# Kernel optimization log

Measured on AMD Instinct MI355X. Metric: run time of the kernel, lower is better.

The kernel has to match this reference:

```python
import jax, jax.numpy as jnp
import numpy as np
import math

EMBED_DIM = 1024
NUM_HEADS = 16
HEAD_DIM = EMBED_DIM // NUM_HEADS


def setup_inputs() -> dict:
    key = jax.random.key(0)
    ks = jax.random.split(key, 12)
    B, N = 2, 2048
    s = 1.0 / math.sqrt(EMBED_DIM)
    inp = {
        "query": jax.random.normal(ks[0], (B, N, EMBED_DIM), jnp.float32),
        "key": jax.random.normal(ks[1], (B, N, EMBED_DIM), jnp.float32),
        "value": jax.random.normal(ks[2], (B, N, EMBED_DIM), jnp.float32),
        "Wq": jax.random.normal(ks[3], (EMBED_DIM, EMBED_DIM), jnp.float32) * s,
        "bq": jnp.zeros((EMBED_DIM,), jnp.float32),
        "Wk": jax.random.normal(ks[4], (EMBED_DIM, EMBED_DIM), jnp.float32) * s,
        "bk": jnp.zeros((EMBED_DIM,), jnp.float32),
        "Wv": jax.random.normal(ks[5], (EMBED_DIM, EMBED_DIM), jnp.float32) * s,
        "bv": jnp.zeros((EMBED_DIM,), jnp.float32),
        "Wo": jax.random.normal(ks[6], (EMBED_DIM, EMBED_DIM), jnp.float32) * s,
        "bo": jnp.zeros((EMBED_DIM,), jnp.float32),
        "gate": jnp.zeros((NUM_HEADS,), jnp.float32),
    }
    return inp


def reference(query, key, value, Wq, bq, Wk, bk, Wv, bv, Wo, bo, gate):
    B, Nq, _ = query.shape
    Nk = key.shape[1]
    H, D = NUM_HEADS, HEAD_DIM
    # projections (Linear: x @ W.T + b); split heads -> [B, H, N, D]
    q = (query @ Wq.T + bq).reshape(B, Nq, H, D).transpose(0, 2, 1, 3)
    k = (key @ Wk.T + bk).reshape(B, Nk, H, D).transpose(0, 2, 1, 3)
    v = (value @ Wv.T + bv).reshape(B, Nk, H, D).transpose(0, 2, 1, 3)
    # scaled logits with per-head sigmoid gate folded into the scale
    scale = jax.nn.sigmoid(gate) / math.sqrt(D)  # [H]
    logits = jnp.einsum("bhqd,bhkd->bhqk", q, k) * scale[None, :, None, None]
    attn = jax.nn.softmax(logits, axis=-1)
    out = jnp.einsum("bhqk,bhkd->bhqd", attn, v)
    out = out.transpose(0, 2, 1, 3).reshape(B, Nq, H * D)
    return out @ Wo.T + bo
```

## Files before the change

kernel.cpp:

```cpp
#include <hip/hip_runtime.h>
#include <hip/hip_bf16.h>
#include <cstdint>


#define DEV __device__ __forceinline__
typedef __attribute__((ext_vector_type(8))) short bf16x8;
typedef __attribute__((ext_vector_type(4))) float f32x4;
typedef unsigned short u16;

DEV void async16(const void* g, void* l) {
  __builtin_amdgcn_global_load_lds(
      (const __attribute__((address_space(1))) unsigned int*)g,
      (__attribute__((address_space(3))) unsigned int*)l, 16, 0, 0);
}

DEV u16 bf16_rne(float f) {
  unsigned int u = __builtin_bit_cast(unsigned int, f);
  u += 0x7FFFu + ((u >> 16) & 1u);
  return (u16)(u >> 16);
}

DEV u16 cvt16(float x) {
  __hip_bfloat16 h = __float2bfloat16(x);
  return __builtin_bit_cast(u16, h);
}

DEV unsigned cvtpk(float lo, float hi) {
  unsigned r;
  asm("v_cvt_pk_bf16_f32 %0, %1, %2" : "=v"(r) : "v"(lo), "v"(hi));
  return r;
}

__global__ __launch_bounds__(256) void cast_all(
    const float* __restrict__ q, const float* __restrict__ k, const float* __restrict__ v,
    const float* __restrict__ Wq, const float* __restrict__ Wk,
    const float* __restrict__ Wv, const float* __restrict__ Wo,
    u16* __restrict__ XQ, u16* __restrict__ XK, u16* __restrict__ XV,
    u16* __restrict__ WQB, u16* __restrict__ WKB, u16* __restrict__ WVB,
    u16* __restrict__ WOB) {
  int idx = blockIdx.x * 256 + threadIdx.x;
  const float* src; u16* dst; int i;
  if      (idx <  524288) { src = q;  dst = XQ;  i = idx; }
  else if (idx < 1048576) { src = k;  dst = XK;  i = idx -  524288; }
  else if (idx < 1572864) { src = v;  dst = XV;  i = idx - 1048576; }
  else if (idx < 1703936) { src = Wq; dst = WQB; i = idx - 1572864; }
  else if (idx < 1835008) { src = Wk; dst = WKB; i = idx - 1703936; }
  else if (idx < 1966080) { src = Wv; dst = WVB; i = idx - 1835008; }
  else                    { src = Wo; dst = WOB; i = idx - 1966080; }
  const float4* p = (const float4*)src + (size_t)i * 2;
  float4 a = p[0], b = p[1];
  union { u16 us[8]; uint4 vv; } u;
  u.us[0] = bf16_rne(a.x); u.us[1] = bf16_rne(a.y);
  u.us[2] = bf16_rne(a.z); u.us[3] = bf16_rne(a.w);
  u.us[4] = bf16_rne(b.x); u.us[5] = bf16_rne(b.y);
  u.us[6] = bf16_rne(b.z); u.us[7] = bf16_rne(b.w);
  ((uint4*)dst)[i] = u.vv;
}

__global__ __launch_bounds__(256, 3) void gemm_qkv(
    const u16* __restrict__ XQ, const u16* __restrict__ XK, const u16* __restrict__ XV,
    const u16* __restrict__ Wb,
    const float* __restrict__ bq, const float* __restrict__ bkb, const float* __restrict__ bv,
    const float* __restrict__ gate,
    u16* __restrict__ QB, u16* __restrict__ KB, u16* __restrict__ VTB) {
  __shared__ __attribute__((aligned(16))) u16 As[2][128 * 32];
  __shared__ __attribute__((aligned(16))) u16 Bs[2][128 * 32];
  const int t = threadIdx.x, lane = t & 63, w = t >> 6;
  const int l15 = lane & 15, quad = lane >> 4;
  const int xcd = blockIdx.x & 7, idx = blockIdx.x >> 3;
  const int seg = idx >> 5, r5 = idx & 31;
  const int bm = (xcd << 2) + (r5 >> 3), bn = r5 & 7;
  const int m0 = bm << 7, n0 = bn << 7;
  const u16* A = (seg == 0) ? XQ : (seg == 1) ? XK : XV;
  const u16* W = Wb + (long)seg * 1048576;
  const int wm = (w >> 1) << 6, wn = (w & 1) << 6;
  const int r0 = t >> 2, cc0 = (t & 3) * 8;
  const u16* gA0 = A + (long)(m0 + r0) * 1024 + cc0;
  const u16* gA1 = gA0 + 64 * 1024;
  const u16* gB0 = W + (long)(n0 + r0) * 1024 + cc0;
  const u16* gB1 = gB0 + 64 * 1024;

  async16(gA0, &As[0][t * 8]); async16(gA1, &As[0][(t + 256) * 8]);
  async16(gB0, &Bs[0][t * 8]); async16(gB1, &Bs[0][(t + 256) * 8]);

  f32x4 acc[4][4] = {};
  for (int k0 = 0; k0 < 1024; k0 += 32) {
    const int cur = (k0 >> 5) & 1;
    __syncthreads();
    if (k0 + 32 < 1024) {
      const int kn = k0 + 32, nb = cur ^ 1;
      async16(gA0 + kn, &As[nb][t * 8]); async16(gA1 + kn, &As[nb][(t + 256) * 8]);
      async16(gB0 + kn, &Bs[nb][t * 8]); async16(gB1 + kn, &Bs[nb][(t + 256) * 8]);
    }
    bf16x8 af[4], bfm[4];
#pragma unroll
    for (int i = 0; i < 4; i++)
      af[i] = *(const bf16x8*)&As[cur][(wm + i * 16 + l15) * 32 + quad * 8];
#pragma unroll
    for (int j = 0; j < 4; j++)
      bfm[j] = *(const bf16x8*)&Bs[cur][(wn + j * 16 + l15) * 32 + quad * 8];
#pragma unroll
    for (int i = 0; i < 4; i++)
#pragma unroll
      for (int j = 0; j < 4; j++)
        acc[i][j] = __builtin_amdgcn_mfma_f32_16x16x32_bf16(af[i], bfm[j], acc[i][j], 0, 0, 0);
  }

  if (seg == 2) {
#pragma unroll
    for (int i = 0; i < 4; i++) {
      int token = m0 + wm + i * 16 + quad * 4;
      int bb_ = token >> 11, n = token & 2047;
#pragma unroll
      for (int j = 0; j < 4; j++) {
        int col = n0 + wn + j * 16 + l15;
        float bb = bv[col];
        union { u16 us[4]; uint2 u2; } pk;
#pragma unroll
        for (int r = 0; r < 4; r++) pk.us[r] = bf16_rne(acc[i][j][r] + bb);
        *(uint2*)&VTB[(long)(bb_ * 1024 + col) * 2048 + n] = pk.u2;
      }
    }
  } else {
    const float* bias = seg ? bkb : bq;
    u16* C = seg ? KB : QB;
#pragma unroll
    for (int j = 0; j < 4; j++) {
      int col = n0 + wn + j * 16 + l15;
      float bb = bias[col];
      float scl = 1.f;
      if (seg == 0) {
        float g = gate[col >> 6];
        float sig = 1.f / (1.f + __builtin_amdgcn_exp2f(-g * 1.44269504f));
        scl = sig * 0.125f * 1.44269504f;
      }
#pragma unroll
      for (int i = 0; i < 4; i++) {
        int row = m0 + wm + i * 16 + quad * 4;
#pragma unroll
        for (int r = 0; r < 4; r++)
          C[(long)(row + r) * 1024 + col] = bf16_rne((acc[i][j][r] + bb) * scl);
      }
    }
  }
}

__global__ __launch_bounds__(256, 2) void gemm_out(
    const u16* __restrict__ A, const u16* __restrict__ W,
    const float* __restrict__ bias, float* __restrict__ Cf) {
  __shared__ __attribute__((aligned(16))) u16 As[2][64 * 32];
  __shared__ __attribute__((aligned(16))) u16 Bs[2][128 * 32];
  const int t = threadIdx.x, lane = t & 63, w = t >> 6;
  const int l15 = lane & 15, quad = lane >> 4;
  const int xcd = blockIdx.x & 7, idx = blockIdx.x >> 3;
  const int bm = (xcd << 3) + (idx >> 3), bn = idx & 7;
  const int m0 = bm << 6, n0 = bn << 7;
  const int wm = (w >> 1) << 5, wn = (w & 1) << 6;
  const int r0 = t >> 2, cc0 = (t & 3) * 8;
  const u16* gA = A + (long)(m0 + r0) * 1024 + cc0;
  const u16* gB0 = W + (long)(n0 + r0) * 1024 + cc0;
  const u16* gB1 = gB0 + 64 * 1024;

  async16(gA, &As[0][t * 8]);
  async16(gB0, &Bs[0][t * 8]); async16(gB1, &Bs[0][(t + 256) * 8]);

  f32x4 acc[2][4] = {};
  for (int k0 = 0; k0 < 1024; k0 += 32) {
    const int cur = (k0 >> 5) & 1;
    __syncthreads();
    if (k0 + 32 < 1024) {
      const int kn = k0 + 32, nb = cur ^ 1;
      async16(gA + kn, &As[nb][t * 8]);
      async16(gB0 + kn, &Bs[nb][t * 8]); async16(gB1 + kn, &Bs[nb][(t + 256) * 8]);
    }
    bf16x8 af[2], bfm[4];
#pragma unroll
    for (int i = 0; i < 2; i++)
      af[i] = *(const bf16x8*)&As[cur][(wm + i * 16 + l15) * 32 + quad * 8];
#pragma unroll
    for (int j = 0; j < 4; j++)
      bfm[j] = *(const bf16x8*)&Bs[cur][(wn + j * 16 + l15) * 32 + quad * 8];
#pragma unroll
    for (int i = 0; i < 2; i++)
#pragma unroll
      for (int j = 0; j < 4; j++)
        acc[i][j] = __builtin_amdgcn_mfma_f32_16x16x32_bf16(af[i], bfm[j], acc[i][j], 0, 0, 0);
  }

#pragma unroll
  for (int j = 0; j < 4; j++) {
    int col = n0 + wn + j * 16 + l15;
    float bb = bias[col];
#pragma unroll
    for (int i = 0; i < 2; i++) {
      int row = m0 + wm + i * 16 + quad * 4;
#pragma unroll
      for (int r = 0; r < 4; r++)
        Cf[(long)(row + r) * 1024 + col] = acc[i][j][r] + bb;
    }
  }
}

__global__ __launch_bounds__(128, 5) void attn_kernel(
    const u16* __restrict__ Q, const u16* __restrict__ Kb,
    const u16* __restrict__ Vt, u16* __restrict__ Op0, u16* __restrict__ Op3,
    float* __restrict__ lp) {
  __shared__ __attribute__((aligned(16))) u16 Ks[2][32 * 64];
  __shared__ __attribute__((aligned(16))) u16 Vs[2][64 * 32];
  const int t = threadIdx.x, lane = t & 63, w = t >> 6;
  const int l15 = lane & 15, quad = lane >> 4;
  const int qt = blockIdx.x >> 2, ksp = blockIdx.x & 3;
  const int h = blockIdx.y, b = blockIdx.z;
  const int q0 = qt * 64, tok0 = b * 2048, key0 = ksp * 512;
  const u16* Kbase = Kb + (long)tok0 * 1024 + h * 64;
  const u16* Vbase = Vt + (long)(b * 1024 + h * 64) * 2048 + key0;

  bf16x8 aq[2][2];
#pragma unroll
  for (int i = 0; i < 2; i++) {
    long row = tok0 + q0 + w * 32 + i * 16 + l15;
#pragma unroll
    for (int ks = 0; ks < 2; ks++)
      aq[i][ks] = *(const bf16x8*)&Q[row * 1024 + h * 64 + ks * 32 + quad * 8];
  }

#pragma unroll
  for (int i = 0; i < 2; i++) {
    int c = i * 128 + t;
    int rk = c >> 3, ck = c & 7, cks = ck ^ ((rk >> 1) & 7);
    async16(&Kbase[(long)(key0 + rk) * 1024 + cks * 8], &Ks[0][c * 8]);
    int rv = c >> 2, cv = c & 3, cvs = cv ^ ((rv >> 1) & 3);
    async16(&Vbase[(long)rv * 2048 + cvs * 8], &Vs[0][c * 8]);
  }

  float l_st[2] = {};
  f32x4 O[2][4] = {};

  for (int kt = 0; kt < 16; kt++) {
    const int cur = kt & 1;
    __syncthreads();
    if (kt + 1 < 16) {
      const int kk = (kt + 1) * 32, nb = cur ^ 1;
#pragma unroll
      for (int i = 0; i < 2; i++) {
        int c = i * 128 + t;
        int rk = c >> 3, ck = c & 7, cks = ck ^ ((rk >> 1) & 7);
        async16(&Kbase[(long)(key0 + kk + rk) * 1024 + cks * 8], &Ks[nb][c * 8]);
        int rv = c >> 2, cv = c & 3, cvs = cv ^ ((rv >> 1) & 3);
        async16(&Vbase[(long)rv * 2048 + kk + cvs * 8], &Vs[nb][c * 8]);
      }
    }

    f32x4 s[2][2] = {};
    __builtin_amdgcn_s_setprio(1);
#pragma unroll
    for (int ks = 0; ks < 2; ks++) {
      bf16x8 bk_[2];
#pragma unroll
      for (int j = 0; j < 2; j++) {
        int rl = 2 * l15 + j;
        bk_[j] = *(const bf16x8*)&Ks[cur][rl * 64 + (((ks * 4 + quad) ^ (l15 & 7))) * 8];
      }
#pragma unroll
      for (int i = 0; i < 2; i++)
#pragma unroll
        for (int j = 0; j < 2; j++)
          s[i][j] = __builtin_amdgcn_mfma_f32_16x16x32_bf16(bk_[j], aq[i][ks], s[i][j], 0, 0, 0);
    }
    __builtin_amdgcn_s_setprio(0);

    bf16x8 ap[2];
#pragma unroll
    for (int i = 0; i < 2; i++) {
      union { unsigned uw[4]; bf16x8 v8; } pw;
#pragma unroll
      for (int r = 0; r < 4; r++) {
        float p0 = __builtin_amdgcn_exp2f(s[i][0][r]);
        float p1 = __builtin_amdgcn_exp2f(s[i][1][r]);
        l_st[i] += p0 + p1;
        pw.uw[r] = cvtpk(p0, p1);
      }
      ap[i] = pw.v8;
    }

    bf16x8 bv_[4];
#pragma unroll
    for (int dj = 0; dj < 4; dj++) {
      int rl = dj * 16 + l15;
      bv_[dj] = *(const bf16x8*)&Vs[cur][rl * 32 + ((quad ^ ((rl >> 1) & 3))) * 8];
    }
    __builtin_amdgcn_s_setprio(1);
#pragma unroll
    for (int i = 0; i < 2; i++)
#pragma unroll
      for (int dj = 0; dj < 4; dj++)
        O[i][dj] = __builtin_amdgcn_mfma_f32_16x16x32_bf16(ap[i], bv_[dj], O[i][dj], 0, 0, 0);
    __builtin_amdgcn_s_setprio(0);
  }

  u16* dst = (ksp == 3) ? Op3 : (Op0 + (long)ksp * 4194304);
#pragma unroll
  for (int i = 0; i < 2; i++) {
    float ls = l_st[i];
    ls += __shfl_xor(ls, 16); ls += __shfl_xor(ls, 32);
    if (quad == 0) {
      long qrow = tok0 + q0 + w * 32 + i * 16 + l15;
      lp[ksp * 65536 + (int)qrow * 16 + h] = ls;
    }
#pragma unroll
    for (int r = 0; r < 4; r++) {
      long row = tok0 + q0 + w * 32 + i * 16 + quad * 4 + r;
#pragma unroll
      for (int dj = 0; dj < 4; dj++)
        dst[row * 1024 + h * 64 + dj * 16 + l15] = cvt16(O[i][dj][r]);
    }
  }
}

__global__ __launch_bounds__(256) void merge_kernel(
    const u16* __restrict__ Op0, const u16* __restrict__ Op3,
    const float* __restrict__ lp, u16* __restrict__ AO) {
  int idx = blockIdx.x * 256 + threadIdx.x;
  int tok = idx >> 7, rem = idx & 127, h = rem >> 3;
  int li = tok * 16 + h;
  float inv = 1.f / (lp[li] + lp[65536 + li] + lp[131072 + li] + lp[196608 + li]);
  union U { uint4 v; u16 us[8]; };
  U a0, a1, a2, a3, uo;
  a0.v = ((const uint4*)Op0)[idx];
  a1.v = ((const uint4*)Op0)[idx + 524288];
  a2.v = ((const uint4*)Op0)[idx + 1048576];
  a3.v = ((const uint4*)Op3)[idx];
#pragma unroll
  for (int j = 0; j < 8; j++) {
    float f0 = __builtin_bit_cast(float, (unsigned)((unsigned)a0.us[j] << 16));
    float f1 = __builtin_bit_cast(float, (unsigned)((unsigned)a1.us[j] << 16));
    float f2 = __builtin_bit_cast(float, (unsigned)((unsigned)a2.us[j] << 16));
    float f3 = __builtin_bit_cast(float, (unsigned)((unsigned)a3.us[j] << 16));
    uo.us[j] = cvt16((f0 + f1 + f2 + f3) * inv);
  }
  ((uint4*)AO)[idx] = uo.v;
}

extern "C" void kernel_launch(void* const* d_in, const int* in_sizes, int n_in,
                              void* d_out, int out_size, void* d_ws, size_t ws_size,
                              hipStream_t stream) {
  const float* q  = (const float*)d_in[0];
  const float* k  = (const float*)d_in[1];
  const float* v  = (const float*)d_in[2];
  const float* Wq = (const float*)d_in[3];
  const float* bq = (const float*)d_in[4];
  const float* Wk = (const float*)d_in[5];
  const float* bk = (const float*)d_in[6];
  const float* Wv = (const float*)d_in[7];
  const float* bv = (const float*)d_in[8];
  const float* Wo = (const float*)d_in[9];
  const float* bo = (const float*)d_in[10];
  const float* gate = (const float*)d_in[11];
  float* out = (float*)d_out;
  char* ws = (char*)d_ws;

  const size_t MB = 1u << 20;
  u16* WQB = (u16*)(ws + 0 * MB);
  u16* WKB = (u16*)(ws + 2 * MB);
  u16* WVB = (u16*)(ws + 4 * MB);
  u16* WOB = (u16*)(ws + 6 * MB);
  u16* XQ  = (u16*)(ws + 8 * MB);
  u16* XK  = (u16*)(ws + 16 * MB);
  u16* XV  = (u16*)(ws + 24 * MB);
  u16* QB  = (u16*)(ws + 32 * MB);
  u16* KB  = (u16*)(ws + 40 * MB);
  u16* OPp  = (u16*)(ws + 8 * MB);
  u16* OPd3 = (u16*)((char*)d_out + 8 * MB);
  float* LP = (float*)(ws + 0 * MB);
  u16* AOB  = (u16*)(ws + 8 * MB);
  u16* VTB  = (u16*)d_out;

  cast_all<<<8192, 256, 0, stream>>>(q, k, v, Wq, Wk, Wv, Wo,
                                     XQ, XK, XV, WQB, WKB, WVB, WOB);
  gemm_qkv<<<768, 256, 0, stream>>>(XQ, XK, XV, WQB, bq, bk, bv, gate, QB, KB, VTB);
  attn_kernel<<<dim3(128, 16, 2), 128, 0, stream>>>(QB, KB, VTB, OPp, OPd3, LP);
  merge_kernel<<<2048, 256, 0, stream>>>(OPp, OPd3, LP, AOB);
  gemm_out<<<512, 256, 0, stream>>>(AOB, WOB, bo, out);
}
```

Baseline: 232.6 us.

## Triple-buffer attention K/V loads with explicit vmcnt waits and XCD-aware block mapping

Changes the attention kernel's K/V staging from double to triple buffering, issuing loads two tiles ahead and waiting with explicit s_waitcnt vmcnt counts between raw barriers instead of __syncthreads. Precomputes the per-thread global and LDS addresses once, outside the loop. Remaps blockIdx.x so blocks sharing a key split land on the same XCD, aiming for better L2 reuse of K/V. The extra LDS buffer and the lower launch-bounds occupancy hint (5 to 3) may reduce concurrent blocks per CU.

```diff
diff --git a/kernel.cpp b/kernel.cpp
--- a/kernel.cpp
+++ b/kernel.cpp
@@ -201,15 +201,16 @@
   }
 }
 
-__global__ __launch_bounds__(128, 5) void attn_kernel(
+__global__ __launch_bounds__(128, 3) void attn_kernel(
     const u16* __restrict__ Q, const u16* __restrict__ Kb,
     const u16* __restrict__ Vt, u16* __restrict__ Op0, u16* __restrict__ Op3,
     float* __restrict__ lp) {
-  __shared__ __attribute__((aligned(16))) u16 Ks[2][32 * 64];
-  __shared__ __attribute__((aligned(16))) u16 Vs[2][64 * 32];
+  __shared__ __attribute__((aligned(16))) u16 Ks[3][32 * 64];
+  __shared__ __attribute__((aligned(16))) u16 Vs[3][64 * 32];
   const int t = threadIdx.x, lane = t & 63, w = t >> 6;
   const int l15 = lane & 15, quad = lane >> 4;
-  const int qt = blockIdx.x >> 2, ksp = blockIdx.x & 3;
+  const int xcd = blockIdx.x & 7, rr = blockIdx.x >> 3;
+  const int ksp = xcd >> 1, qt = ((xcd & 1) << 4) | rr;
   const int h = blockIdx.y, b = blockIdx.z;
   const int q0 = qt * 64, tok0 = b * 2048, key0 = ksp * 512;
   const u16* Kbase = Kb + (long)tok0 * 1024 + h * 64;
@@ -224,32 +225,44 @@
       aq[i][ks] = *(const bf16x8*)&Q[row * 1024 + h * 64 + ks * 32 + quad * 8];
   }
 
-#pragma unroll
-  for (int i = 0; i < 2; i++) {
-    int c = i * 128 + t;
-    int rk = c >> 3, ck = c & 7, cks = ck ^ ((rk >> 1) & 7);
-    async16(&Kbase[(long)(key0 + rk) * 1024 + cks * 8], &Ks[0][c * 8]);
-    int rv = c >> 2, cv = c & 3, cvs = cv ^ ((rv >> 1) & 3);
-    async16(&Vbase[(long)rv * 2048 + cvs * 8], &Vs[0][c * 8]);
-  }
+  const int c0 = t, c1 = 128 + t;
+  const int rk0 = c0 >> 3, rk1 = c1 >> 3, rv0 = c0 >> 2, rv1 = c1 >> 2;
+  const u16* kgA = Kbase + (long)(key0 + rk0) * 1024 + ((c0 & 7) ^ ((rk0 >> 1) & 7)) * 8;
+  const u16* kgB = Kbase + (long)(key0 + rk1) * 1024 + ((c1 & 7) ^ ((rk1 >> 1) & 7)) * 8;
+  const u16* vgA = Vbase + (long)rv0 * 2048 + ((c0 & 3) ^ ((rv0 >> 1) & 3)) * 8;
+  const u16* vgB = Vbase + (long)rv1 * 2048 + ((c1 & 3) ^ ((rv1 >> 1) & 3)) * 8;
+  u16* ksA = &Ks[0][c0 * 8];
+  u16* ksB = &Ks[0][c1 * 8];
+  u16* vsA = &Vs[0][c0 * 8];
+  u16* vsB = &Vs[0][c1 * 8];
+
+  auto STAGE = [&](int tk, int bu) {
+    const long ko = (long)tk * 32768;
+    const int vo = tk * 32;
+    async16(kgA + ko, ksA + bu * 2048);
+    async16(kgB + ko, ksB + bu * 2048);
+    async16(vgA + vo, vsA + bu * 2048);
+    async16(vgB + vo, vsB + bu * 2048);
+  };
+
+  STAGE(0, 0); STAGE(1, 1);
 
   float l_st[2] = {};
   f32x4 O[2][4] = {};
+  int cur = 0;
 
   for (int kt = 0; kt < 16; kt++) {
-    const int cur = kt & 1;
-    __syncthreads();
-    if (kt + 1 < 16) {
-      const int kk = (kt + 1) * 32, nb = cur ^ 1;
-#pragma unroll
-      for (int i = 0; i < 2; i++) {
-        int c = i * 128 + t;
-        int rk = c >> 3, ck = c & 7, cks = ck ^ ((rk >> 1) & 7);
-        async16(&Kbase[(long)(key0 + kk + rk) * 1024 + cks * 8], &Ks[nb][c * 8]);
-        int rv = c >> 2, cv = c & 3, cvs = cv ^ ((rv >> 1) & 3);
-        async16(&Vbase[(long)rv * 2048 + kk + cvs * 8], &Vs[nb][c * 8]);
-      }
-    }
+    __builtin_amdgcn_s_barrier();
+    if (kt < 14) {
+      const int nb2 = (cur == 0) ? 2 : cur - 1;
+      STAGE(kt + 2, nb2);
+      asm volatile("s_waitcnt vmcnt(8)" ::: "memory");
+    } else if (kt == 14) {
+      asm volatile("s_waitcnt vmcnt(4)" ::: "memory");
+    } else {
+      asm volatile("s_waitcnt vmcnt(0)" ::: "memory");
+    }
+    __builtin_amdgcn_s_barrier();
 
     f32x4 s[2][2] = {};
     __builtin_amdgcn_s_setprio(1);
@@ -296,6 +309,8 @@
       for (int dj = 0; dj < 4; dj++)
         O[i][dj] = __builtin_amdgcn_mfma_f32_16x16x32_bf16(ap[i], bv_[dj], O[i][dj], 0, 0, 0);
     __builtin_amdgcn_s_setprio(0);
+
+    cur = (cur == 2) ? 0 : cur + 1;
   }
 
   u16* dst = (ksp == 3) ? Op3 : (Op0 + (long)ksp * 4194304);
```

Measured after the change: 234.3 us. About the same (+0.7%).

## Double attention query tile per block to 128 rows with XCD-aware block mapping

Applied to the files above, without the earlier changes.

Attention blocks grow from 128 to 256 threads (four waves), so each block covers 128 query rows. Every staged K/V tile is now shared by twice as many query rows, halving K/V global traffic per query. Block indices are remapped so blocks on the same XCD work on the same key split, which should improve L2 reuse. The staging loads are simplified to one precomputed 16-byte async copy per thread, and the key loop is fully unrolled. The trade-offs are half as many blocks to fill the GPU and a changed launch-bounds occupancy target.

```diff
diff --git a/kernel.cpp b/kernel.cpp
--- a/kernel.cpp
+++ b/kernel.cpp
@@ -201,7 +201,7 @@
   }
 }
 
-__global__ __launch_bounds__(128, 5) void attn_kernel(
+__global__ __launch_bounds__(256, 7) void attn_kernel(
     const u16* __restrict__ Q, const u16* __restrict__ Kb,
     const u16* __restrict__ Vt, u16* __restrict__ Op0, u16* __restrict__ Op3,
     float* __restrict__ lp) {
@@ -209,9 +209,10 @@
   __shared__ __attribute__((aligned(16))) u16 Vs[2][64 * 32];
   const int t = threadIdx.x, lane = t & 63, w = t >> 6;
   const int l15 = lane & 15, quad = lane >> 4;
-  const int qt = blockIdx.x >> 2, ksp = blockIdx.x & 3;
+  const int xcd = blockIdx.x & 7, rr = blockIdx.x >> 3;
+  const int ksp = xcd >> 1, qt = ((xcd & 1) << 3) | rr;
   const int h = blockIdx.y, b = blockIdx.z;
-  const int q0 = qt * 64, tok0 = b * 2048, key0 = ksp * 512;
+  const int q0 = qt * 128, tok0 = b * 2048, key0 = ksp * 512;
   const u16* Kbase = Kb + (long)tok0 * 1024 + h * 64;
   const u16* Vbase = Vt + (long)(b * 1024 + h * 64) * 2048 + key0;
 
@@ -224,32 +225,28 @@
       aq[i][ks] = *(const bf16x8*)&Q[row * 1024 + h * 64 + ks * 32 + quad * 8];
   }
 
-#pragma unroll
-  for (int i = 0; i < 2; i++) {
-    int c = i * 128 + t;
-    int rk = c >> 3, ck = c & 7, cks = ck ^ ((rk >> 1) & 7);
-    async16(&Kbase[(long)(key0 + rk) * 1024 + cks * 8], &Ks[0][c * 8]);
-    int rv = c >> 2, cv = c & 3, cvs = cv ^ ((rv >> 1) & 3);
-    async16(&Vbase[(long)rv * 2048 + cvs * 8], &Vs[0][c * 8]);
-  }
+  const int rk = t >> 3, ck = t & 7;
+  const int rv = t >> 2, cv = t & 3;
+  const u16* kg = Kbase + (long)(key0 + rk) * 1024 + ((ck ^ ((rk >> 1) & 7)) * 8);
+  const u16* vg = Vbase + (long)rv * 2048 + ((cv ^ ((rv >> 1) & 3)) * 8);
+  u16* ksd = &Ks[0][t * 8];
+  u16* vsd = &Vs[0][t * 8];
+
+  auto STAGE = [&](int tk, int bu) {
+    async16(kg + (long)tk * 32768, ksd + bu * 2048);
+    async16(vg + tk * 32, vsd + bu * 2048);
+  };
+
+  STAGE(0, 0);
 
   float l_st[2] = {};
   f32x4 O[2][4] = {};
 
+#pragma unroll
   for (int kt = 0; kt < 16; kt++) {
     const int cur = kt & 1;
     __syncthreads();
-    if (kt + 1 < 16) {
-      const int kk = (kt + 1) * 32, nb = cur ^ 1;
-#pragma unroll
-      for (int i = 0; i < 2; i++) {
-        int c = i * 128 + t;
-        int rk = c >> 3, ck = c & 7, cks = ck ^ ((rk >> 1) & 7);
-        async16(&Kbase[(long)(key0 + kk + rk) * 1024 + cks * 8], &Ks[nb][c * 8]);
-        int rv = c >> 2, cv = c & 3, cvs = cv ^ ((rv >> 1) & 3);
-        async16(&Vbase[(long)rv * 2048 + kk + cvs * 8], &Vs[nb][c * 8]);
-      }
-    }
+    if (kt + 1 < 16) STAGE(kt + 1, cur ^ 1);
 
     f32x4 s[2][2] = {};
     __builtin_amdgcn_s_setprio(1);
@@ -378,7 +375,7 @@
   cast_all<<<8192, 256, 0, stream>>>(q, k, v, Wq, Wk, Wv, Wo,
                                      XQ, XK, XV, WQB, WKB, WVB, WOB);
   gemm_qkv<<<768, 256, 0, stream>>>(XQ, XK, XV, WQB, bq, bk, bv, gate, QB, KB, VTB);
-  attn_kernel<<<dim3(128, 16, 2), 128, 0, stream>>>(QB, KB, VTB, OPp, OPd3, LP);
+  attn_kernel<<<dim3(64, 16, 2), 256, 0, stream>>>(QB, KB, VTB, OPp, OPd3, LP);
   merge_kernel<<<2048, 256, 0, stream>>>(OPp, OPd3, LP, AOB);
   gemm_out<<<512, 256, 0, stream>>>(AOB, WOB, bo, out);
 }
```

Measured after the change: 552.4 us. 2.37x slower.
